# Kernel optimization log

Measured on AMD Instinct MI355X. Metric: run time of the kernel, lower is better.

The kernel has to match this reference:

```python
import jax, jax.numpy as jnp
import numpy as np

EPS = 1e-4

def _ema(unit_embeddings, unit_confidence, unit_mask):
    # unit_embeddings: (B, J, D), unit_confidence/unit_mask: (B, J)
    emb_j = jnp.swapaxes(unit_embeddings, 0, 1)        # (J, B, D)
    p_j = jnp.swapaxes(unit_confidence, 0, 1)          # (J, B)
    m_j = jnp.swapaxes(unit_mask, 0, 1)                # (J, B)

    B, _, D = unit_embeddings.shape
    prev0 = jnp.zeros((B, D), dtype=unit_embeddings.dtype)

    def step(prev, inp):
        emb, p, m = inp                                # (B,D), (B,), (B,)
        p = jnp.clip(p, EPS, 1.0 - EPS)[:, None]       # (B,1)
        m = m[:, None]                                 # (B,1)
        cur = jnp.where(m, emb, jnp.zeros_like(emb))
        new = jnp.where(m, p * cur + (1.0 - p) * prev, prev)
        return new, new

    _, smoothed = jax.lax.scan(step, prev0, (emb_j, p_j, m_j))  # (J, B, D)
    return jnp.swapaxes(smoothed, 0, 1)                # (B, J, D)

def _upsample(smoothed, boundary_mask):
    # smoothed: (B, J, D), boundary_mask: (B, L) bool
    J = smoothed.shape[1]
    idx = jnp.cumsum(boundary_mask.astype(jnp.int32), axis=1) - 1
    idx = jnp.clip(idx, 0, J - 1)                      # (B, L)
    return jnp.take_along_axis(smoothed, idx[:, :, None], axis=1)  # (B, L, D)

def setup_inputs() -> dict:
    key = jax.random.key(0)
    k1, k2, k3, k4 = jax.random.split(key, 4)
    B, J, L, D = 16, 1024, 4096, 512
    unit_embeddings = jax.random.normal(k1, (B, J, D), dtype=jnp.float32)
    unit_confidence = jax.random.uniform(k2, (B, J), dtype=jnp.float32)
    unit_mask = jax.random.randint(k3, (B, J), 0, 2).astype(bool)
    boundary_mask = jax.random.randint(k4, (B, L), 0, 2).astype(bool)
    return {
        "unit_embeddings": unit_embeddings,
        "unit_confidence": unit_confidence,
        "unit_mask": unit_mask,
        "boundary_mask": boundary_mask,
    }

def reference(unit_embeddings, unit_confidence, unit_mask, boundary_mask):
    smoothed = _ema(unit_embeddings, unit_confidence, unit_mask)
    frames = _upsample(smoothed, boundary_mask)
    return frames
```

## Files before the change

kernel.cpp:

```cpp
#include <hip/hip_runtime.h>
#include <cstddef>

namespace {
constexpr int Bn = 16;
constexpr int Jn = 1024;
constexpr int Ln = 4096;
constexpr int Dn = 512;
constexpr int G  = 32;
constexpr int C  = Jn / G;
constexpr float kEps = 1e-4f;
}

__global__ void k_aprod(const float* __restrict__ conf, const int* __restrict__ mask,
                        float* __restrict__ PA, float* __restrict__ Ap) {
  int t = blockIdx.x * blockDim.x + threadIdx.x;
  if (t >= Bn * C) return;
  int b = t / C, c = t % C;
  int base = b * Jn + c * G;
  float prod = 1.0f;
  for (int i = 0; i < G; ++i) {
    float p = conf[base + i];
    p = fminf(fmaxf(p, kEps), 1.0f - kEps);
    float a = (mask[base + i] != 0) ? (1.0f - p) : 1.0f;
    prod *= a;
    PA[base + i] = prod;
  }
  Ap[t] = prod;
}

__global__ void k_idx(const int* __restrict__ bnd, int* __restrict__ idx) {
  int b = blockIdx.x;
  int t = threadIdx.x;
  const int per = Ln / 256;
  const int* row = bnd + (size_t)b * Ln;
  int s = 0;
#pragma unroll
  for (int i = 0; i < per; ++i) s += (row[t * per + i] != 0) ? 1 : 0;

  __shared__ int sh[256];
  sh[t] = s;
  __syncthreads();
  for (int off = 1; off < 256; off <<= 1) {
    int v = (t >= off) ? sh[t - off] : 0;
    __syncthreads();
    sh[t] += v;
    __syncthreads();
  }
  int run = sh[t] - s;
#pragma unroll
  for (int i = 0; i < per; ++i) {
    run += (row[t * per + i] != 0) ? 1 : 0;
    int v = run - 1;
    v = v < 0 ? 0 : (v > Jn - 1 ? Jn - 1 : v);
    idx[(size_t)b * Ln + t * per + i] = v;
  }
}

__global__ void k_chunk_end(const float* __restrict__ emb, const float* __restrict__ conf,
                            const int* __restrict__ mask, float* __restrict__ E) {
  int bc = blockIdx.x;
  int b = bc / C, c = bc % C;
  int d4 = threadIdx.x;
  float4 s = make_float4(0.f, 0.f, 0.f, 0.f);
  for (int i = 0; i < G; ++i) {
    int j = c * G + i;
    float p = conf[b * Jn + j];
    p = fminf(fmaxf(p, kEps), 1.0f - kEps);
    bool m = (mask[b * Jn + j] != 0);
    float4 e = ((const float4*)(emb + ((size_t)(b * Jn + j)) * Dn))[d4];
    if (m) {
      float q = 1.0f - p;
      s.x = p * e.x + q * s.x;
      s.y = p * e.y + q * s.y;
      s.z = p * e.z + q * s.z;
      s.w = p * e.w + q * s.w;
    }
  }
  ((float4*)(E + (size_t)bc * Dn))[d4] = s;
}

__global__ void k_chunk_start(const float* __restrict__ E, const float* __restrict__ Ap,
                              float* __restrict__ S) {
  int t = blockIdx.x * blockDim.x + threadIdx.x;
  if (t >= Bn * (Dn / 4)) return;
  int b = t / (Dn / 4), d4 = t % (Dn / 4);
  float4 s = make_float4(0.f, 0.f, 0.f, 0.f);
  for (int c = 0; c < C; ++c) {
    ((float4*)(S + ((size_t)(b * C + c)) * Dn))[d4] = s;
    float a = Ap[b * C + c];
    float4 e = ((const float4*)(E + ((size_t)(b * C + c)) * Dn))[d4];
    s.x = e.x + a * s.x;
    s.y = e.y + a * s.y;
    s.z = e.z + a * s.z;
    s.w = e.w + a * s.w;
  }
}

__global__ void k_smooth(const float* __restrict__ emb, const float* __restrict__ conf,
                         const int* __restrict__ mask, const float* __restrict__ PA,
                         const float* __restrict__ S, float* __restrict__ smoothed) {
  int bc = blockIdx.x;
  int b = bc / C, c = bc % C;
  int d4 = threadIdx.x;
  float4 s = make_float4(0.f, 0.f, 0.f, 0.f);
  float4 sc = ((const float4*)(S + (size_t)bc * Dn))[d4];
  for (int i = 0; i < G; ++i) {
    int j = c * G + i;
    float p = conf[b * Jn + j];
    p = fminf(fmaxf(p, kEps), 1.0f - kEps);
    bool m = (mask[b * Jn + j] != 0);
    float4 e = ((const float4*)(emb + ((size_t)(b * Jn + j)) * Dn))[d4];
    if (m) {
      float q = 1.0f - p;
      s.x = p * e.x + q * s.x;
      s.y = p * e.y + q * s.y;
      s.z = p * e.z + q * s.z;
      s.w = p * e.w + q * s.w;
    }
    float pa = PA[b * Jn + j];
    float4 o;
    o.x = s.x + pa * sc.x;
    o.y = s.y + pa * sc.y;
    o.z = s.z + pa * sc.z;
    o.w = s.w + pa * sc.w;
    ((float4*)(smoothed + ((size_t)(b * Jn + j)) * Dn))[d4] = o;
  }
}

__global__ void k_gather(const float* __restrict__ smoothed, const int* __restrict__ idx,
                         float* __restrict__ out) {
  size_t tid = (size_t)blockIdx.x * blockDim.x + threadIdx.x;
  int d4 = (int)(tid & (Dn / 4 - 1));
  size_t bl = tid >> 7;
  int j = idx[bl];
  size_t b = bl >> 12;
  float4 v = ((const float4*)(smoothed + (b * Jn + (size_t)j) * Dn))[d4];
  ((float4*)out)[tid] = v;
}

extern "C" void kernel_launch(void* const* d_in, const int* in_sizes, int n_in,
                              void* d_out, int out_size, void* d_ws, size_t ws_size,
                              hipStream_t stream) {
  const float* emb  = (const float*)d_in[0];
  const float* conf = (const float*)d_in[1];
  const int*   mask = (const int*)d_in[2];
  const int*   bnd  = (const int*)d_in[3];
  float* out = (float*)d_out;

  float* ws = (float*)d_ws;
  float* smoothed = ws;
  float* E   = smoothed + (size_t)Bn * Jn * Dn;
  float* S   = E + (size_t)Bn * C * Dn;
  float* PA  = S + (size_t)Bn * C * Dn;
  float* Ap  = PA + (size_t)Bn * Jn;
  int*   idx = (int*)(Ap + Bn * C);

  hipLaunchKernelGGL(k_aprod, dim3((Bn * C + 255) / 256), dim3(256), 0, stream,
                     conf, mask, PA, Ap);
  hipLaunchKernelGGL(k_idx, dim3(Bn), dim3(256), 0, stream, bnd, idx);
  hipLaunchKernelGGL(k_chunk_end, dim3(Bn * C), dim3(Dn / 4), 0, stream,
                     emb, conf, mask, E);
  hipLaunchKernelGGL(k_chunk_start, dim3((Bn * (Dn / 4) + 255) / 256), dim3(256), 0, stream,
                     E, Ap, S);
  hipLaunchKernelGGL(k_smooth, dim3(Bn * C), dim3(Dn / 4), 0, stream,
                     emb, conf, mask, PA, S, smoothed);
  size_t total4 = (size_t)Bn * Ln * (Dn / 4);
  hipLaunchKernelGGL(k_gather, dim3((unsigned)(total4 / 256)), dim3(256), 0, stream,
                     smoothed, idx, out);
}
```

Before: 194.2 us.

## Fuse chunk-local scan with prefix products and apply carry correction in gather

The first pass now computes the chunk-local EMA state, writes it for every position, and also produces the per-position and per-chunk decay products, replacing the separate aprod kernel. The second full pass over the embeddings (k_smooth) is removed. The chunk carry-in correction (local + PA*S) is applied inside the gather kernel instead. This drops one full read of the embeddings and one kernel launch, at the cost of extra PA and S loads in the gather, which processes four times as many rows as there are units.

```diff
diff --git a/kernel.cpp b/kernel.cpp
--- a/kernel.cpp
+++ b/kernel.cpp
@@ -9,23 +9,6 @@
 constexpr int G  = 32;
 constexpr int C  = Jn / G;
 constexpr float kEps = 1e-4f;
-}
-
-__global__ void k_aprod(const float* __restrict__ conf, const int* __restrict__ mask,
-                        float* __restrict__ PA, float* __restrict__ Ap) {
-  int t = blockIdx.x * blockDim.x + threadIdx.x;
-  if (t >= Bn * C) return;
-  int b = t / C, c = t % C;
-  int base = b * Jn + c * G;
-  float prod = 1.0f;
-  for (int i = 0; i < G; ++i) {
-    float p = conf[base + i];
-    p = fminf(fmaxf(p, kEps), 1.0f - kEps);
-    float a = (mask[base + i] != 0) ? (1.0f - p) : 1.0f;
-    prod *= a;
-    PA[base + i] = prod;
-  }
-  Ap[t] = prod;
 }
 
 __global__ void k_idx(const int* __restrict__ bnd, int* __restrict__ idx) {
@@ -56,27 +39,35 @@
   }
 }
 
-__global__ void k_chunk_end(const float* __restrict__ emb, const float* __restrict__ conf,
-                            const int* __restrict__ mask, float* __restrict__ E) {
+__global__ void k_pass1(const float* __restrict__ emb, const float* __restrict__ conf,
+                        const int* __restrict__ mask, float* __restrict__ local,
+                        float* __restrict__ E, float* __restrict__ PA,
+                        float* __restrict__ Ap) {
   int bc = blockIdx.x;
   int b = bc / C, c = bc % C;
   int d4 = threadIdx.x;
+  int base = b * Jn + c * G;
   float4 s = make_float4(0.f, 0.f, 0.f, 0.f);
+  float prod = 1.0f;
   for (int i = 0; i < G; ++i) {
-    int j = c * G + i;
-    float p = conf[b * Jn + j];
+    int j = base + i;
+    float p = conf[j];
     p = fminf(fmaxf(p, kEps), 1.0f - kEps);
-    bool m = (mask[b * Jn + j] != 0);
-    float4 e = ((const float4*)(emb + ((size_t)(b * Jn + j)) * Dn))[d4];
+    bool m = (mask[j] != 0);
+    float q = 1.0f - p;
+    float4 e = ((const float4*)(emb + (size_t)j * Dn))[d4];
     if (m) {
-      float q = 1.0f - p;
       s.x = p * e.x + q * s.x;
       s.y = p * e.y + q * s.y;
       s.z = p * e.z + q * s.z;
       s.w = p * e.w + q * s.w;
+      prod *= q;
     }
+    ((float4*)(local + (size_t)j * Dn))[d4] = s;
+    if (d4 == 0) PA[j] = prod;
   }
   ((float4*)(E + (size_t)bc * Dn))[d4] = s;
+  if (d4 == 0) Ap[bc] = prod;
 }
 
 __global__ void k_chunk_start(const float* __restrict__ E, const float* __restrict__ Ap,
@@ -96,46 +87,24 @@
   }
 }
 
-__global__ void k_smooth(const float* __restrict__ emb, const float* __restrict__ conf,
-                         const int* __restrict__ mask, const float* __restrict__ PA,
-                         const float* __restrict__ S, float* __restrict__ smoothed) {
-  int bc = blockIdx.x;
-  int b = bc / C, c = bc % C;
-  int d4 = threadIdx.x;
-  float4 s = make_float4(0.f, 0.f, 0.f, 0.f);
-  float4 sc = ((const float4*)(S + (size_t)bc * Dn))[d4];
-  for (int i = 0; i < G; ++i) {
-    int j = c * G + i;
-    float p = conf[b * Jn + j];
-    p = fminf(fmaxf(p, kEps), 1.0f - kEps);
-    bool m = (mask[b * Jn + j] != 0);
-    float4 e = ((const float4*)(emb + ((size_t)(b * Jn + j)) * Dn))[d4];
-    if (m) {
-      float q = 1.0f - p;
-      s.x = p * e.x + q * s.x;
-      s.y = p * e.y + q * s.y;
-      s.z = p * e.z + q * s.z;
-      s.w = p * e.w + q * s.w;
-    }
-    float pa = PA[b * Jn + j];
-    float4 o;
-    o.x = s.x + pa * sc.x;
-    o.y = s.y + pa * sc.y;
-    o.z = s.z + pa * sc.z;
-    o.w = s.w + pa * sc.w;
-    ((float4*)(smoothed + ((size_t)(b * Jn + j)) * Dn))[d4] = o;
-  }
-}
-
-__global__ void k_gather(const float* __restrict__ smoothed, const int* __restrict__ idx,
+__global__ void k_gather(const float* __restrict__ local, const float* __restrict__ PA,
+                         const float* __restrict__ S, const int* __restrict__ idx,
                          float* __restrict__ out) {
   size_t tid = (size_t)blockIdx.x * blockDim.x + threadIdx.x;
   int d4 = (int)(tid & (Dn / 4 - 1));
   size_t bl = tid >> 7;
   int j = idx[bl];
   size_t b = bl >> 12;
-  float4 v = ((const float4*)(smoothed + (b * Jn + (size_t)j) * Dn))[d4];
-  ((float4*)out)[tid] = v;
+  int c = j >> 5;
+  float pa = PA[b * Jn + (size_t)j];
+  float4 sc = ((const float4*)(S + (b * C + (size_t)c) * Dn))[d4];
+  float4 lo = ((const float4*)(local + (b * Jn + (size_t)j) * Dn))[d4];
+  float4 o;
+  o.x = lo.x + pa * sc.x;
+  o.y = lo.y + pa * sc.y;
+  o.z = lo.z + pa * sc.z;
+  o.w = lo.w + pa * sc.w;
+  ((float4*)out)[tid] = o;
 }
 
 extern "C" void kernel_launch(void* const* d_in, const int* in_sizes, int n_in,
@@ -148,23 +117,19 @@
   float* out = (float*)d_out;
 
   float* ws = (float*)d_ws;
-  float* smoothed = ws;
-  float* E   = smoothed + (size_t)Bn * Jn * Dn;
+  float* local = ws;
+  float* E   = local + (size_t)Bn * Jn * Dn;
   float* S   = E + (size_t)Bn * C * Dn;
   float* PA  = S + (size_t)Bn * C * Dn;
   float* Ap  = PA + (size_t)Bn * Jn;
   int*   idx = (int*)(Ap + Bn * C);
 
-  hipLaunchKernelGGL(k_aprod, dim3((Bn * C + 255) / 256), dim3(256), 0, stream,
-                     conf, mask, PA, Ap);
   hipLaunchKernelGGL(k_idx, dim3(Bn), dim3(256), 0, stream, bnd, idx);
-  hipLaunchKernelGGL(k_chunk_end, dim3(Bn * C), dim3(Dn / 4), 0, stream,
-                     emb, conf, mask, E);
+  hipLaunchKernelGGL(k_pass1, dim3(Bn * C), dim3(Dn / 4), 0, stream,
+                     emb, conf, mask, local, E, PA, Ap);
   hipLaunchKernelGGL(k_chunk_start, dim3((Bn * (Dn / 4) + 255) / 256), dim3(256), 0, stream,
                      E, Ap, S);
-  hipLaunchKernelGGL(k_smooth, dim3(Bn * C), dim3(Dn / 4), 0, stream,
-                     emb, conf, mask, PA, S, smoothed);
   size_t total4 = (size_t)Bn * Ln * (Dn / 4);
   hipLaunchKernelGGL(k_gather, dim3((unsigned)(total4 / 256)), dim3(256), 0, stream,
-                     smoothed, idx, out);
+                     local, PA, S, idx, out);
 }
```

Result: faster. 187.6 us (-3.4%).
